# Kernel tuning notes

Measured on AMD Instinct MI355X. Metric: run time of the kernel, lower is better.

Reference implementation:

```python
import jax, jax.numpy as jnp
import numpy as np

N_NODES = 100000
N_EDGES = 800000


def gcn_conv(x, W, b, src, dst, ew, n):
    # PyG GCNConv with edge weights and self-loops already included in (src, dst, ew):
    # deg[i] = sum of incoming edge weights at i; norm_e = d^-1/2[src] * w_e * d^-1/2[dst]
    h = x @ W                                                  # [N, F_out]
    deg = jax.ops.segment_sum(ew, dst, num_segments=n)         # [N]
    dinv = jnp.where(deg > 0, jax.lax.rsqrt(deg), 0.0)
    norm = dinv[src] * ew * dinv[dst]                          # [E]
    out = jax.ops.segment_sum(h[src] * norm[:, None], dst, num_segments=n)
    return out + b


def add_self_loops(edge_index, edge_weight, n):
    loop = jnp.arange(n, dtype=edge_index.dtype)
    src = jnp.concatenate([edge_index[0], loop])
    dst = jnp.concatenate([edge_index[1], loop])
    ew = jnp.concatenate([edge_weight, jnp.ones((n,), edge_weight.dtype)])
    return src, dst, ew


def setup_inputs() -> dict:
    key = jax.random.key(0)
    ks = jax.random.split(key, 10)
    x = jax.random.normal(ks[0], (N_NODES, 5), jnp.float32)
    edge_index = jax.random.randint(ks[1], (2, N_EDGES), 0, N_NODES, dtype=jnp.int64)
    edge_weight = jax.random.uniform(ks[2], (N_EDGES,), jnp.float32)
    def glorot(k, fan_in, fan_out):
        s = float(np.sqrt(6.0 / (fan_in + fan_out)))
        return jax.random.uniform(k, (fan_in, fan_out), jnp.float32, -s, s)
    return {
        "x": x,
        "edge_index": edge_index,
        "edge_weight": edge_weight,
        "W1": glorot(ks[3], 5, 320),
        "b1": jnp.zeros((320,), jnp.float32),
        "W2": glorot(ks[4], 320, 160),
        "b2": jnp.zeros((160,), jnp.float32),
        "We": glorot(ks[5], 160, 80),
        "be": jnp.zeros((80,), jnp.float32),
    }


def reference(x, edge_index, edge_weight, W1, b1, W2, b2, We, be):
    n = x.shape[0]
    src, dst, ew = add_self_loops(edge_index, edge_weight, n)
    h = gcn_conv(x, W1, b1, src, dst, ew, n)        # conv1
    h = jax.nn.relu(h)
    h = gcn_conv(h, W2, b2, src, dst, ew, n)        # conv2
    return h @ We + be                              # embed linear
```

## Files before the change

kernel.cpp:

```cpp
#include <hip/hip_runtime.h>

#define NF0 5
#define F1 320
#define F2 160
#define F3 80
#define NSUB 8
#define SUBCAP 512

typedef float f32x4 __attribute__((ext_vector_type(4)));
typedef _Float16 f16x8 __attribute__((ext_vector_type(8)));


__global__ void k_prep(int padz, int* __restrict__ zreg, int zwords,
                       const float* __restrict__ W2, const float* __restrict__ We,
                       _Float16* __restrict__ Bh,
                       const float* __restrict__ b2, const float* __restrict__ be,
                       float* __restrict__ bc,
                       const unsigned int* __restrict__ ei32, int E, int* __restrict__ flag) {
    __shared__ int ok;
    int b = blockIdx.x;
    if (b < padz) {
        int t = b * 256 + threadIdx.x;
        if (t < zwords) zreg[t] = 0;
        return;
    }
    b -= padz;
    if (b < 100) {
        int t = b * 256 + threadIdx.x;
        if (t < 25600) {
            int fid = t >> 9;
            int rem = t & 511;
            int lane = rem >> 3, i = rem & 7;
            int kk = fid / 5, ct = fid - kk * 5;
            int col = ct * 16 + (lane & 15);
            int row = kk * 32 + (lane >> 4) * 8 + i;
            const float* wr = W2 + (size_t)row * F2;
            float acc = 0.f;
            #pragma unroll 4
            for (int m = 0; m < F2; m += 4) {
                float4 w4 = *(const float4*)(wr + m);
                acc += w4.x * We[m * F3 + col] + w4.y * We[(m + 1) * F3 + col]
                     + w4.z * We[(m + 2) * F3 + col] + w4.w * We[(m + 3) * F3 + col];
            }
            Bh[((size_t)fid * 64 + lane) * 8 + i] = (_Float16)acc;
        }
    } else if (b == 100) {
        int j = threadIdx.x;
        if (j < F3) {
            float s = be[j];
            for (int k = 0; k < F2; ++k) s += b2[k] * We[k * F3 + j];
            bc[j] = s;
        }
    } else {
        if (threadIdx.x == 0) ok = 1;
        __syncthreads();
        int npairs = E < 2048 ? E : 2048;
        for (int i = threadIdx.x; i < npairs; i += blockDim.x)
            if (ei32[2 * i + 1] != 0u) ok = 0;
        __syncthreads();
        if (threadIdx.x == 0) *flag = ok;
    }
}


__global__ void k_binA(const void* ei, const float* __restrict__ ew, const int* __restrict__ flag,
                       int* __restrict__ bin_cnt , int2* __restrict__ bins,
                       int n_bins, int* __restrict__ ovf_n, int* __restrict__ ovf,
                       int ovf_cap, int E) {
    int e = blockIdx.x * blockDim.x + threadIdx.x;
    if (e >= E) return;
    int sub = blockIdx.x & (NSUB - 1);
    int s, d;
    if (*flag) {
        const long long* p = (const long long*)ei;
        s = (int)p[e]; d = (int)p[E + e];
    } else {
        const int* p = (const int*)ei;
        s = p[e]; d = p[E + e];
    }
    float w = ew[e];
    int b = d >> 8;
    int pos = atomicAdd(&bin_cnt[(sub * n_bins + b) * 4], 1);
    if (pos < SUBCAP) {
        int2 pk;
        pk.x = s | ((d & 255) << 24);
        pk.y = __float_as_int(w);
        bins[(size_t)b * (NSUB * SUBCAP) + sub * SUBCAP + pos] = pk;
    } else {
        int o = atomicAdd(ovf_n, 1);
        if (o < ovf_cap) {
            ovf[3 * o] = s; ovf[3 * o + 1] = d; ovf[3 * o + 2] = __float_as_int(w);
        }
    }
}


__global__ __launch_bounds__(512) void k_binB1(const int2* __restrict__ bins,
                                               const int* __restrict__ bin_cnt, int n_bins,
                                               float* __restrict__ dinv,
                                               const int* __restrict__ ovf_n,
                                               const int* __restrict__ ovf, int ovf_cap, int N) {
    __shared__ float deg_l[256];
    int b = blockIdx.x, t = threadIdx.x;
    if (t < 256) deg_l[t] = 0.f;
    __syncthreads();
    int th = t >> 8;
    int tt = t & 255;
    for (int sp = 0; sp < NSUB; sp += 2) {
        int sub = sp + th;
        int ne = bin_cnt[(sub * n_bins + b) * 4]; if (ne > SUBCAP) ne = SUBCAP;
        const int2* bp = bins + (size_t)b * (NSUB * SUBCAP) + sub * SUBCAP;
        for (int j = tt; j < ne; j += 256) {
            int2 pk = bp[j];
            atomicAdd(&deg_l[((unsigned int)pk.x) >> 24], __int_as_float(pk.y));
        }
    }
    int n = *ovf_n; if (n > ovf_cap) n = ovf_cap;
    int lo = b * 256;
    for (int j = t; j < n; j += 512) {
        int d = ovf[3 * j + 1];
        if (d >= lo && d < lo + 256)
            atomicAdd(&deg_l[d - lo], __int_as_float(ovf[3 * j + 2]));
    }
    __syncthreads();
    int node = lo + t;
    if (t < 256 && node < N) dinv[node] = rsqrtf(1.0f + deg_l[t]);
}


__global__ __launch_bounds__(512) void k_binB2(const int2* __restrict__ bins,
                                               const int* __restrict__ bin_cnt, int n_bins,
                                               const float* __restrict__ dinv,
                                               const float* __restrict__ x,
                                               int* __restrict__ cnt, int2* __restrict__ bucket,
                                               int cap, float* __restrict__ agg1,
                                               int* __restrict__ ovf_n, int* __restrict__ ovf,
                                               int ovf_cap, int N) {
    __shared__ int cnt_l[256];
    __shared__ float acc_l[256 * NF0];
    int b = blockIdx.x, t = threadIdx.x;
    if (t < 256) cnt_l[t] = 0;
    for (int q = t; q < 256 * NF0; q += 512) acc_l[q] = 0.f;
    int nsnap = *ovf_n; if (nsnap > ovf_cap) nsnap = ovf_cap;
    __syncthreads();
    int lo = b * 256;

    for (int j = t; j < nsnap; j += 512) {
        int d = ovf[3 * j + 1];
        if (d >= lo && d < lo + 256) {
            int s = ovf[3 * j];
            float w = __int_as_float(ovf[3 * j + 2]) * dinv[s];
            const float* xs = x + (size_t)s * NF0;
            int dl = d - lo;
            #pragma unroll
            for (int f = 0; f < NF0; ++f)
                atomicAdd(&acc_l[dl * NF0 + f], xs[f] * w);
        }
    }

    int th = t >> 8;
    int tt = t & 255;
    for (int sp = 0; sp < NSUB; sp += 2) {
        int sub = sp + th;
        int ne = bin_cnt[(sub * n_bins + b) * 4]; if (ne > SUBCAP) ne = SUBCAP;
        const int2* bp = bins + (size_t)b * (NSUB * SUBCAP) + sub * SUBCAP;
        for (int j = tt; j < ne; j += 256) {
            int2 pk = bp[j];
            int s = pk.x & 0xFFFFFF;
            int dl = ((unsigned int)pk.x) >> 24;
            int node = lo + dl;
            int pos = atomicAdd(&cnt_l[dl], 1);
            if (pos < cap) {
                int2 out_pk; out_pk.x = s; out_pk.y = pk.y;
                bucket[(size_t)node * cap + pos] = out_pk;
            } else {
                int o = atomicAdd(ovf_n, 1);
                if (o < ovf_cap) { ovf[3 * o] = s; ovf[3 * o + 1] = node; ovf[3 * o + 2] = pk.y; }
            }
            float w = __int_as_float(pk.y) * dinv[s];
            const float* xs = x + (size_t)s * NF0;
            float4 sv = *(const float4*)xs;
            float s4 = xs[4];
            atomicAdd(&acc_l[dl * NF0 + 0], sv.x * w);
            atomicAdd(&acc_l[dl * NF0 + 1], sv.y * w);
            atomicAdd(&acc_l[dl * NF0 + 2], sv.z * w);
            atomicAdd(&acc_l[dl * NF0 + 3], sv.w * w);
            atomicAdd(&acc_l[dl * NF0 + 4], s4 * w);
        }
    }
    __syncthreads();

    int node = lo + t;
    if (t < 256 && node < N) {
        float di = dinv[node];
        float sc = di * di;
        const float* xn = x + (size_t)node * NF0;
        float* op = agg1 + (size_t)node * NF0;
        #pragma unroll
        for (int f = 0; f < NF0; ++f)
            op[f] = di * acc_l[t * NF0 + f] + sc * xn[f];
        int c = cnt_l[t]; if (c > cap) c = cap;
        cnt[node] = c;
    }
}


__global__ __launch_bounds__(512) void k_node(const float* __restrict__ agg1,
                                              const float* __restrict__ W1,
                                              const float* __restrict__ b1,
                                              const _Float16* __restrict__ Bh,
                                              const float* __restrict__ dinv,
                                              _Float16* __restrict__ g, int N) {
    __shared__ float W_l[6 * F1];
    __shared__ _Float16 B_l[50 * 64 * 8];
    int tid = threadIdx.x;
    if (tid < 480) {
        float4 v = (tid < 400) ? ((const float4*)W1)[tid] : ((const float4*)b1)[tid - 400];
        ((float4*)W_l)[tid] = v;
    }
    {
        const float4* src = (const float4*)Bh;
        float4* dst = (float4*)B_l;
        for (int i = tid; i < 3200; i += 512) dst[i] = src[i];
    }
    __syncthreads();

    int w = tid >> 6, l = tid & 63;
    int nl = l & 15, kg = l >> 4;
    int base = blockIdx.x * 128 + w * 16;
    int n0 = base + nl;

    float a0v[5] = {0.f, 0.f, 0.f, 0.f, 0.f};
    if (n0 < N) {
        const float* ap = agg1 + (size_t)n0 * NF0;
        #pragma unroll
        for (int j = 0; j < 5; ++j) a0v[j] = ap[j];
    }

    f32x4 zero = {0.f, 0.f, 0.f, 0.f};
    f32x4 acc[5] = {zero, zero, zero, zero, zero};
    const f16x8* blp = (const f16x8*)B_l;

    #pragma unroll
    for (int kk = 0; kk < 10; ++kk) {
        int k0 = kk * 32 + kg * 8;
        float v0[8];
        const float* bb = W_l + 5 * F1 + k0;
        #pragma unroll
        for (int i = 0; i < 8; ++i) v0[i] = bb[i];
        #pragma unroll
        for (int j = 0; j < 5; ++j) {
            const float* wp = W_l + j * F1 + k0;
            float aj0 = a0v[j];
            #pragma unroll
            for (int i = 0; i < 8; ++i) v0[i] += aj0 * wp[i];
        }
        f16x8 ah0;
        #pragma unroll
        for (int i = 0; i < 8; ++i)
            ah0[i] = (_Float16)fmaxf(v0[i], 0.f);
        #pragma unroll
        for (int ct = 0; ct < 5; ++ct) {
            f16x8 bf = blp[(kk * 5 + ct) * 64 + l];
            acc[ct] = __builtin_amdgcn_mfma_f32_16x16x32_f16(ah0, bf, acc[ct], 0, 0, 0);
        }
    }

    #pragma unroll
    for (int r = 0; r < 4; ++r) {
        int r0 = base + kg * 4 + r;
        if (r0 < N) {
            float dv = dinv[r0];
            #pragma unroll
            for (int ct = 0; ct < 5; ++ct)
                g[(size_t)r0 * F3 + ct * 16 + nl] = (_Float16)(acc[ct][r] * dv);
        }
    }
}


__global__ __launch_bounds__(256) void k_aggB(const _Float16* __restrict__ g,
                                              const float* __restrict__ dinv,
                                              const float* __restrict__ bc,
                                              const int* __restrict__ cnt,
                                              const int2* __restrict__ bucket, int cap,
                                              float* __restrict__ out, int N) {
    int t = blockIdx.x * blockDim.x + threadIdx.x;
    if (t >= 10 * N) return;
    int i = t / 10;
    int c = (t - i * 10) << 3;
    float acc[8];
    #pragma unroll
    for (int e = 0; e < 8; ++e) acc[e] = 0.f;
    int cn = cnt[i];
    const int4* row4 = (const int4*)(bucket + (size_t)i * cap);
    int j = 0;
    for (; j + 2 <= cn; j += 2) {
        int4 q = row4[j >> 1];
        float w0 = __int_as_float(q.y);
        float w1 = __int_as_float(q.w);
        f16x8 a0 = *(const f16x8*)(g + (size_t)q.x * F3 + c);
        f16x8 a1 = *(const f16x8*)(g + (size_t)q.z * F3 + c);
        #pragma unroll
        for (int e = 0; e < 8; ++e)
            acc[e] += (float)a0[e] * w0 + (float)a1[e] * w1;
    }
    if (j < cn) {
        int2 p0 = ((const int2*)row4)[j];
        float w0 = __int_as_float(p0.y);
        f16x8 a0 = *(const f16x8*)(g + (size_t)p0.x * F3 + c);
        #pragma unroll
        for (int e = 0; e < 8; ++e)
            acc[e] += (float)a0[e] * w0;
    }
    float di = dinv[i];
    f16x8 u0 = *(const f16x8*)(g + (size_t)i * F3 + c);
    const float4* bp = (const float4*)(bc + c);
    float4 q0 = bp[0], q1 = bp[1];
    float4 o0, o1;
    o0.x = di * (acc[0] + (float)u0[0]) + q0.x;
    o0.y = di * (acc[1] + (float)u0[1]) + q0.y;
    o0.z = di * (acc[2] + (float)u0[2]) + q0.z;
    o0.w = di * (acc[3] + (float)u0[3]) + q0.w;
    o1.x = di * (acc[4] + (float)u0[4]) + q1.x;
    o1.y = di * (acc[5] + (float)u0[5]) + q1.y;
    o1.z = di * (acc[6] + (float)u0[6]) + q1.z;
    o1.w = di * (acc[7] + (float)u0[7]) + q1.w;
    float4* op = (float4*)(out + (size_t)i * F3 + c);
    op[0] = o0; op[1] = o1;
}

__global__ void k_fixB(const _Float16* __restrict__ g, const float* __restrict__ dinv,
                       const int* __restrict__ ovf_n, const int* __restrict__ ovf, int ovf_cap,
                       float* __restrict__ out) {
    int n = *ovf_n; if (n > ovf_cap) n = ovf_cap;
    for (int j = blockIdx.x * blockDim.x + threadIdx.x; j < n; j += gridDim.x * blockDim.x) {
        int s = ovf[3 * j], d = ovf[3 * j + 1];
        float w = dinv[d] * __int_as_float(ovf[3 * j + 2]);
        for (int f = 0; f < F3; ++f)
            atomicAdd(&out[(size_t)d * F3 + f], (float)g[(size_t)s * F3 + f] * w);
    }
}


static inline size_t align256(size_t x) { return (x + 255) & ~(size_t)255; }

extern "C" void kernel_launch(void* const* d_in, const int* in_sizes, int n_in,
                              void* d_out, int out_size, void* d_ws, size_t ws_size,
                              hipStream_t stream) {
    const float* x  = (const float*)d_in[0];
    const void*  ei = d_in[1];
    const float* ew = (const float*)d_in[2];
    const float* W1 = (const float*)d_in[3];
    const float* b1 = (const float*)d_in[4];
    const float* W2 = (const float*)d_in[5];
    const float* b2 = (const float*)d_in[6];
    const float* We = (const float*)d_in[7];
    const float* be = (const float*)d_in[8];
    float* out = (float*)d_out;

    int N = in_sizes[0] / NF0;
    int E = in_sizes[2];

    const int OVF_CAP = 131072;
    int n_bins = (N + 255) >> 8;

    char* p = (char*)d_ws;
    auto alloc = [&](size_t bytes) { char* r = p; p += align256(bytes); return r; };
    int*   flag  = (int*)alloc(4);
    int zwords = 16 + NSUB * n_bins * 4;
    int*   zreg  = (int*)alloc((size_t)zwords * 4);
    int*   ovf_n = zreg;
    int*   bin_cnt = zreg + 16;
    float* dinv  = (float*)alloc((size_t)N * 4);
    int*   cnt   = (int*)  alloc((size_t)N * 4);
    int*   ovf   = (int*)  alloc((size_t)OVF_CAP * 12);
    int2*  bins  = (int2*) alloc((size_t)n_bins * NSUB * SUBCAP * 8);
    float* agg1  = (float*)alloc((size_t)N * NF0 * 4);
    float* bc    = (float*)alloc((size_t)F3 * 4);
    _Float16* Bh = (_Float16*)alloc((size_t)50 * 64 * 8 * 2);
    _Float16* g  = (_Float16*)alloc((size_t)N * F3 * 2);

    size_t used = (size_t)(p - (char*)d_ws);
    int cap = 24;
    if (ws_size > used) {
        size_t avail = (ws_size - used) / ((size_t)N * 8);
        if (avail < (size_t)cap) cap = (int)avail;
    } else cap = 4;
    if (cap < 4) cap = 4;
    int2* bucket = (int2*)alloc((size_t)N * cap * 8);

    int eb   = (E + 255) / 256;
    int padz = (zwords + 255) / 256;

    k_prep<<<padz + 102, 256, 0, stream>>>(padz, zreg, zwords, W2, We, Bh, b2, be, bc,
                                           (const unsigned int*)ei, E, flag);

    k_binA<<<eb, 256, 0, stream>>>(ei, ew, flag, bin_cnt, bins, n_bins, ovf_n, ovf, OVF_CAP, E);
    k_binB1<<<n_bins, 512, 0, stream>>>(bins, bin_cnt, n_bins, dinv, ovf_n, ovf, OVF_CAP, N);
    k_binB2<<<n_bins, 512, 0, stream>>>(bins, bin_cnt, n_bins, dinv, x, cnt, bucket, cap,
                                        agg1, ovf_n, ovf, OVF_CAP, N);

    k_node<<<(N + 127) / 128, 512, 0, stream>>>(agg1, W1, b1, Bh, dinv, g, N);
    k_aggB<<<(10 * N + 255) / 256, 256, 0, stream>>>(g, dinv, bc, cnt, bucket, cap, out, N);
    k_fixB<<<16, 256, 0, stream>>>(g, dinv, ovf_n, ovf, OVF_CAP, out);
}
```

Baseline: 156.5 us.

## Fuse node transform into binning kernel and move weight prep into degree kernel

The per-node layer-1 linear, ReLU and MFMA product with the folded W2·We matrix now runs inside the bucket-building kernel, using the aggregated features kept in shared memory. This removes the agg1 global buffer and one kernel launch. The W2·We folding and bias prep move from the init kernel into extra blocks of the degree kernel, so the init kernel only zeroes counters. Output stores in the final aggregation become nontemporal. The cost is that each of the fewer, larger blocks must load W1 and Bh into shared memory, which raises shared-memory use and may lower occupancy of the binning kernel.

```diff
diff --git a/kernel.cpp b/kernel.cpp
--- a/kernel.cpp
+++ b/kernel.cpp
@@ -11,51 +11,16 @@
 typedef _Float16 f16x8 __attribute__((ext_vector_type(8)));
 
 
-__global__ void k_prep(int padz, int* __restrict__ zreg, int zwords,
-                       const float* __restrict__ W2, const float* __restrict__ We,
-                       _Float16* __restrict__ Bh,
-                       const float* __restrict__ b2, const float* __restrict__ be,
-                       float* __restrict__ bc,
+__global__ void k_init(int* __restrict__ zreg, int zwords,
                        const unsigned int* __restrict__ ei32, int E, int* __restrict__ flag) {
-    __shared__ int ok;
-    int b = blockIdx.x;
-    if (b < padz) {
-        int t = b * 256 + threadIdx.x;
-        if (t < zwords) zreg[t] = 0;
-        return;
-    }
-    b -= padz;
-    if (b < 100) {
-        int t = b * 256 + threadIdx.x;
-        if (t < 25600) {
-            int fid = t >> 9;
-            int rem = t & 511;
-            int lane = rem >> 3, i = rem & 7;
-            int kk = fid / 5, ct = fid - kk * 5;
-            int col = ct * 16 + (lane & 15);
-            int row = kk * 32 + (lane >> 4) * 8 + i;
-            const float* wr = W2 + (size_t)row * F2;
-            float acc = 0.f;
-            #pragma unroll 4
-            for (int m = 0; m < F2; m += 4) {
-                float4 w4 = *(const float4*)(wr + m);
-                acc += w4.x * We[m * F3 + col] + w4.y * We[(m + 1) * F3 + col]
-                     + w4.z * We[(m + 2) * F3 + col] + w4.w * We[(m + 3) * F3 + col];
-            }
-            Bh[((size_t)fid * 64 + lane) * 8 + i] = (_Float16)acc;
-        }
-    } else if (b == 100) {
-        int j = threadIdx.x;
-        if (j < F3) {
-            float s = be[j];
-            for (int k = 0; k < F2; ++k) s += b2[k] * We[k * F3 + j];
-            bc[j] = s;
-        }
-    } else {
+    for (int t = blockIdx.x * 256 + threadIdx.x; t < zwords; t += gridDim.x * 256)
+        zreg[t] = 0;
+    if (blockIdx.x == 0) {
+        __shared__ int ok;
         if (threadIdx.x == 0) ok = 1;
         __syncthreads();
-        int npairs = E < 2048 ? E : 2048;
-        for (int i = threadIdx.x; i < npairs; i += blockDim.x)
+        int np = E < 2048 ? E : 2048;
+        for (int i = threadIdx.x; i < np; i += 256)
             if (ei32[2 * i + 1] != 0u) ok = 0;
         __syncthreads();
         if (threadIdx.x == 0) *flag = ok;
@@ -95,13 +60,47 @@
 }
 
 
-__global__ __launch_bounds__(512) void k_binB1(const int2* __restrict__ bins,
-                                               const int* __restrict__ bin_cnt, int n_bins,
-                                               float* __restrict__ dinv,
-                                               const int* __restrict__ ovf_n,
-                                               const int* __restrict__ ovf, int ovf_cap, int N) {
+__global__ __launch_bounds__(512) void k_binB1x(const int2* __restrict__ bins,
+                                                const int* __restrict__ bin_cnt, int n_bins,
+                                                float* __restrict__ dinv,
+                                                const int* __restrict__ ovf_n,
+                                                const int* __restrict__ ovf, int ovf_cap, int N,
+                                                const float* __restrict__ W2,
+                                                const float* __restrict__ We,
+                                                _Float16* __restrict__ Bh,
+                                                const float* __restrict__ b2,
+                                                const float* __restrict__ be,
+                                                float* __restrict__ bc) {
     __shared__ float deg_l[256];
     int b = blockIdx.x, t = threadIdx.x;
+    if (b >= n_bins) {
+        int xb = b - n_bins;
+        if (xb < 50) {
+            int idx = xb * 512 + t;
+            int fid = idx >> 9;
+            int rem = idx & 511;
+            int lane = rem >> 3, i = rem & 7;
+            int kk = fid / 5, ct = fid - kk * 5;
+            int col = ct * 16 + (lane & 15);
+            int row = kk * 32 + (lane >> 4) * 8 + i;
+            const float* wr = W2 + (size_t)row * F2;
+            float acc = 0.f;
+            #pragma unroll 4
+            for (int m = 0; m < F2; m += 4) {
+                float4 w4 = *(const float4*)(wr + m);
+                acc += w4.x * We[m * F3 + col] + w4.y * We[(m + 1) * F3 + col]
+                     + w4.z * We[(m + 2) * F3 + col] + w4.w * We[(m + 3) * F3 + col];
+            }
+            Bh[((size_t)fid * 64 + lane) * 8 + i] = (_Float16)acc;
+        } else {
+            if (t < F3) {
+                float s = be[t];
+                for (int k = 0; k < F2; ++k) s += b2[k] * We[k * F3 + t];
+                bc[t] = s;
+            }
+        }
+        return;
+    }
     if (t < 256) deg_l[t] = 0.f;
     __syncthreads();
     int th = t >> 8;
@@ -128,17 +127,33 @@
 }
 
 
-__global__ __launch_bounds__(512) void k_binB2(const int2* __restrict__ bins,
-                                               const int* __restrict__ bin_cnt, int n_bins,
-                                               const float* __restrict__ dinv,
-                                               const float* __restrict__ x,
-                                               int* __restrict__ cnt, int2* __restrict__ bucket,
-                                               int cap, float* __restrict__ agg1,
-                                               int* __restrict__ ovf_n, int* __restrict__ ovf,
-                                               int ovf_cap, int N) {
+__global__ __launch_bounds__(512) void k_binB2node(const int2* __restrict__ bins,
+                                                   const int* __restrict__ bin_cnt, int n_bins,
+                                                   const float* __restrict__ dinv,
+                                                   const float* __restrict__ x,
+                                                   const float* __restrict__ W1,
+                                                   const float* __restrict__ b1,
+                                                   const _Float16* __restrict__ Bh,
+                                                   int* __restrict__ cnt,
+                                                   int2* __restrict__ bucket, int cap,
+                                                   int* __restrict__ ovf_n, int* __restrict__ ovf,
+                                                   int ovf_cap,
+                                                   _Float16* __restrict__ g, int N) {
     __shared__ int cnt_l[256];
     __shared__ float acc_l[256 * NF0];
+    __shared__ float W_l[6 * F1];
+    __shared__ _Float16 B_l[50 * 64 * 8];
     int b = blockIdx.x, t = threadIdx.x;
+
+    if (t < 480) {
+        float4 v = (t < 400) ? ((const float4*)W1)[t] : ((const float4*)b1)[t - 400];
+        ((float4*)W_l)[t] = v;
+    }
+    {
+        const float4* src = (const float4*)Bh;
+        float4* dst = (float4*)B_l;
+        for (int i = t; i < 3200; i += 512) dst[i] = src[i];
+    }
     if (t < 256) cnt_l[t] = 0;
     for (int q = t; q < 256 * NF0; q += 512) acc_l[q] = 0.f;
     int nsnap = *ovf_n; if (nsnap > ovf_cap) nsnap = ovf_cap;
@@ -190,90 +205,67 @@
     }
     __syncthreads();
 
-    int node = lo + t;
-    if (t < 256 && node < N) {
-        float di = dinv[node];
+    int node0 = lo + t;
+    if (t < 256 && node0 < N) {
+        float di = dinv[node0];
         float sc = di * di;
-        const float* xn = x + (size_t)node * NF0;
-        float* op = agg1 + (size_t)node * NF0;
+        const float* xn = x + (size_t)node0 * NF0;
         #pragma unroll
         for (int f = 0; f < NF0; ++f)
-            op[f] = di * acc_l[t * NF0 + f] + sc * xn[f];
+            acc_l[t * NF0 + f] = di * acc_l[t * NF0 + f] + sc * xn[f];
         int c = cnt_l[t]; if (c > cap) c = cap;
-        cnt[node] = c;
-    }
-}
-
-
-__global__ __launch_bounds__(512) void k_node(const float* __restrict__ agg1,
-                                              const float* __restrict__ W1,
-                                              const float* __restrict__ b1,
-                                              const _Float16* __restrict__ Bh,
-                                              const float* __restrict__ dinv,
-                                              _Float16* __restrict__ g, int N) {
-    __shared__ float W_l[6 * F1];
-    __shared__ _Float16 B_l[50 * 64 * 8];
-    int tid = threadIdx.x;
-    if (tid < 480) {
-        float4 v = (tid < 400) ? ((const float4*)W1)[tid] : ((const float4*)b1)[tid - 400];
-        ((float4*)W_l)[tid] = v;
-    }
-    {
-        const float4* src = (const float4*)Bh;
-        float4* dst = (float4*)B_l;
-        for (int i = tid; i < 3200; i += 512) dst[i] = src[i];
-    }
-    __syncthreads();
-
-    int w = tid >> 6, l = tid & 63;
+        cnt[node0] = c;
+    }
+    __syncthreads();
+
+    int w = t >> 6, l = t & 63;
     int nl = l & 15, kg = l >> 4;
-    int base = blockIdx.x * 128 + w * 16;
-    int n0 = base + nl;
-
-    float a0v[5] = {0.f, 0.f, 0.f, 0.f, 0.f};
-    if (n0 < N) {
-        const float* ap = agg1 + (size_t)n0 * NF0;
-        #pragma unroll
-        for (int j = 0; j < 5; ++j) a0v[j] = ap[j];
-    }
-
     f32x4 zero = {0.f, 0.f, 0.f, 0.f};
-    f32x4 acc[5] = {zero, zero, zero, zero, zero};
     const f16x8* blp = (const f16x8*)B_l;
 
     #pragma unroll
-    for (int kk = 0; kk < 10; ++kk) {
-        int k0 = kk * 32 + kg * 8;
-        float v0[8];
-        const float* bb = W_l + 5 * F1 + k0;
-        #pragma unroll
-        for (int i = 0; i < 8; ++i) v0[i] = bb[i];
-        #pragma unroll
-        for (int j = 0; j < 5; ++j) {
-            const float* wp = W_l + j * F1 + k0;
-            float aj0 = a0v[j];
-            #pragma unroll
-            for (int i = 0; i < 8; ++i) v0[i] += aj0 * wp[i];
-        }
-        f16x8 ah0;
-        #pragma unroll
-        for (int i = 0; i < 8; ++i)
-            ah0[i] = (_Float16)fmaxf(v0[i], 0.f);
-        #pragma unroll
-        for (int ct = 0; ct < 5; ++ct) {
-            f16x8 bf = blp[(kk * 5 + ct) * 64 + l];
-            acc[ct] = __builtin_amdgcn_mfma_f32_16x16x32_f16(ah0, bf, acc[ct], 0, 0, 0);
-        }
-    }
-
-    #pragma unroll
-    for (int r = 0; r < 4; ++r) {
-        int r0 = base + kg * 4 + r;
-        if (r0 < N) {
-            float dv = dinv[r0];
-            #pragma unroll
-            for (int ct = 0; ct < 5; ++ct)
-                g[(size_t)r0 * F3 + ct * 16 + nl] = (_Float16)(acc[ct][r] * dv);
+    for (int set = 0; set < 2; ++set) {
+        int nlocal = w * 32 + set * 16 + nl;
+        int base = lo + w * 32 + set * 16;
+        float a0v[5];
+        #pragma unroll
+        for (int j = 0; j < 5; ++j) a0v[j] = acc_l[nlocal * NF0 + j];
+
+        f32x4 acc[5] = {zero, zero, zero, zero, zero};
+        #pragma unroll
+        for (int kk = 0; kk < 10; ++kk) {
+            int k0 = kk * 32 + kg * 8;
+            float v0[8];
+            const float* bb = W_l + 5 * F1 + k0;
+            #pragma unroll
+            for (int i = 0; i < 8; ++i) v0[i] = bb[i];
+            #pragma unroll
+            for (int j = 0; j < 5; ++j) {
+                const float* wp = W_l + j * F1 + k0;
+                float aj0 = a0v[j];
+                #pragma unroll
+                for (int i = 0; i < 8; ++i) v0[i] += aj0 * wp[i];
+            }
+            f16x8 ah0;
+            #pragma unroll
+            for (int i = 0; i < 8; ++i)
+                ah0[i] = (_Float16)fmaxf(v0[i], 0.f);
+            #pragma unroll
+            for (int ct = 0; ct < 5; ++ct) {
+                f16x8 bf = blp[(kk * 5 + ct) * 64 + l];
+                acc[ct] = __builtin_amdgcn_mfma_f32_16x16x32_f16(ah0, bf, acc[ct], 0, 0, 0);
+            }
+        }
+
+        #pragma unroll
+        for (int r = 0; r < 4; ++r) {
+            int r0 = base + kg * 4 + r;
+            if (r0 < N) {
+                float dv = dinv[r0];
+                #pragma unroll
+                for (int ct = 0; ct < 5; ++ct)
+                    g[(size_t)r0 * F3 + ct * 16 + nl] = (_Float16)(acc[ct][r] * dv);
+            }
         }
     }
 }
@@ -315,9 +307,9 @@
     }
     float di = dinv[i];
     f16x8 u0 = *(const f16x8*)(g + (size_t)i * F3 + c);
-    const float4* bp = (const float4*)(bc + c);
-    float4 q0 = bp[0], q1 = bp[1];
-    float4 o0, o1;
+    const f32x4* bp = (const f32x4*)(bc + c);
+    f32x4 q0 = bp[0], q1 = bp[1];
+    f32x4 o0, o1;
     o0.x = di * (acc[0] + (float)u0[0]) + q0.x;
     o0.y = di * (acc[1] + (float)u0[1]) + q0.y;
     o0.z = di * (acc[2] + (float)u0[2]) + q0.z;
@@ -326,8 +318,9 @@
     o1.y = di * (acc[5] + (float)u0[5]) + q1.y;
     o1.z = di * (acc[6] + (float)u0[6]) + q1.z;
     o1.w = di * (acc[7] + (float)u0[7]) + q1.w;
-    float4* op = (float4*)(out + (size_t)i * F3 + c);
-    op[0] = o0; op[1] = o1;
+    f32x4* op = (f32x4*)(out + (size_t)i * F3 + c);
+    __builtin_nontemporal_store(o0, op);
+    __builtin_nontemporal_store(o1, op + 1);
 }
 
 __global__ void k_fixB(const _Float16* __restrict__ g, const float* __restrict__ dinv,
@@ -376,7 +369,6 @@
     int*   cnt   = (int*)  alloc((size_t)N * 4);
     int*   ovf   = (int*)  alloc((size_t)OVF_CAP * 12);
     int2*  bins  = (int2*) alloc((size_t)n_bins * NSUB * SUBCAP * 8);
-    float* agg1  = (float*)alloc((size_t)N * NF0 * 4);
     float* bc    = (float*)alloc((size_t)F3 * 4);
     _Float16* Bh = (_Float16*)alloc((size_t)50 * 64 * 8 * 2);
     _Float16* g  = (_Float16*)alloc((size_t)N * F3 * 2);
@@ -387,21 +379,19 @@
         size_t avail = (ws_size - used) / ((size_t)N * 8);
         if (avail < (size_t)cap) cap = (int)avail;
     } else cap = 4;
+    cap &= ~1;
     if (cap < 4) cap = 4;
     int2* bucket = (int2*)alloc((size_t)N * cap * 8);
 
     int eb   = (E + 255) / 256;
-    int padz = (zwords + 255) / 256;
-
-    k_prep<<<padz + 102, 256, 0, stream>>>(padz, zreg, zwords, W2, We, Bh, b2, be, bc,
-                                           (const unsigned int*)ei, E, flag);
-
+    int zb   = (zwords + 255) / 256;
+
+    k_init<<<zb, 256, 0, stream>>>(zreg, zwords, (const unsigned int*)ei, E, flag);
     k_binA<<<eb, 256, 0, stream>>>(ei, ew, flag, bin_cnt, bins, n_bins, ovf_n, ovf, OVF_CAP, E);
-    k_binB1<<<n_bins, 512, 0, stream>>>(bins, bin_cnt, n_bins, dinv, ovf_n, ovf, OVF_CAP, N);
-    k_binB2<<<n_bins, 512, 0, stream>>>(bins, bin_cnt, n_bins, dinv, x, cnt, bucket, cap,
-                                        agg1, ovf_n, ovf, OVF_CAP, N);
-
-    k_node<<<(N + 127) / 128, 512, 0, stream>>>(agg1, W1, b1, Bh, dinv, g, N);
+    k_binB1x<<<n_bins + 51, 512, 0, stream>>>(bins, bin_cnt, n_bins, dinv, ovf_n, ovf, OVF_CAP, N,
+                                              W2, We, Bh, b2, be, bc);
+    k_binB2node<<<n_bins, 512, 0, stream>>>(bins, bin_cnt, n_bins, dinv, x, W1, b1, Bh,
+                                            cnt, bucket, cap, ovf_n, ovf, OVF_CAP, g, N);
     k_aggB<<<(10 * N + 255) / 256, 256, 0, stream>>>(g, dinv, bc, cnt, bucket, cap, out, N);
     k_fixB<<<16, 256, 0, stream>>>(g, dinv, ovf_n, ovf, OVF_CAP, out);
 }
```

Result: slower. 161.1 us (+3.0%).
